# Kernel optimization log

Measured on AMD Instinct MI355X. Metric: run time of the kernel, lower is better.

The kernel has to match this reference:

```python
import jax, jax.numpy as jnp
import numpy as np

D = 128      # feature_dim
EMO = 25     # emotion_dim
DMM = 58     # _3dmm_dim
T = 512      # sequence length
BS = 16      # speaker batch
REP = 4      # repeat_interleave
NL = 3       # lstm layers
P_WEIGHT = 1e-5


def _lin(key, out_d, in_d):
    k1, k2 = jax.random.split(key)
    s = 1.0 / np.sqrt(in_d)
    W = jax.random.uniform(k1, (out_d, in_d), minval=-s, maxval=s, dtype=jnp.float32)
    b = jax.random.uniform(k2, (out_d,), minval=-s, maxval=s, dtype=jnp.float32)
    return W, b


def setup_inputs() -> dict:
    key = jax.random.key(0)
    ks = jax.random.split(key, 24)
    B = BS * REP
    inp = {
        'speaker_emotion': jax.random.normal(ks[0], (BS, T, EMO), jnp.float32),
        'listener_emotion': jax.random.normal(ks[1], (B, T, EMO), jnp.float32),
        'speaker_3dmm': jax.random.normal(ks[2], (BS, T, DMM), jnp.float32),
        'listener_3dmm': jax.random.normal(ks[3], (B, T, DMM), jnp.float32),
        'person_specific_factor': jax.random.normal(ks[4], (BS, D), jnp.float32),
        'repeat_interleave': REP,
    }
    specs = [('W_em', 'b_em', D, EMO), ('W_3d', 'b_3d', D, DMM),
             ('Wq_e', 'bq_e', D, D), ('Wk_e', 'bk_e', D, D), ('Wv_e', 'bv_e', D, D),
             ('Wq_d', 'bq_d', D, D), ('Wk_d', 'bk_d', D, D), ('Wv_d', 'bv_d', D, D),
             ('W_fus', 'b_fus', D, 2 * D), ('W_fc1', 'b_fc1', D, D), ('W_fc2', 'b_fc2', 1, D)]
    for i, (wn, bn, o, ii) in enumerate(specs):
        W, b = _lin(ks[5 + i], o, ii)
        inp[wn] = W
        inp[bn] = b
    # stacked 3-layer LSTM params, torch gate order (i, f, g, o)
    kL = jax.random.split(ks[5 + len(specs)], 4)
    s = 1.0 / np.sqrt(D)
    inp['W_ih'] = jax.random.uniform(kL[0], (NL, 4 * D, D), minval=-s, maxval=s, dtype=jnp.float32)
    inp['W_hh'] = jax.random.uniform(kL[1], (NL, 4 * D, D), minval=-s, maxval=s, dtype=jnp.float32)
    inp['b_ih'] = jax.random.uniform(kL[2], (NL, 4 * D), minval=-s, maxval=s, dtype=jnp.float32)
    inp['b_hh'] = jax.random.uniform(kL[3], (NL, 4 * D), minval=-s, maxval=s, dtype=jnp.float32)
    return inp


def _cross_attn(y, x, Wq, bq, Wk, bk, Wv, bv):
    # queries from listener features y [b,q,d]; keys/values from speaker x [b,k,d]
    q = y @ Wq.T + bq
    k = x @ Wk.T + bk
    v = x @ Wv.T + bv
    attn = jax.nn.softmax(jnp.einsum('bqd,bkd->bqk', q, k) / np.sqrt(D), axis=-1)
    return jnp.einsum('bqk,bkd->bqd', attn, v)


def _lstm_flat(flat, W_ih, W_hh, b_ih, b_hh):
    # faithful replication of the per-timestep torch loop: one 3-layer LSTM
    # over the flattened (t-major, b-minor) sequence, batch size 1.
    def step(carry, x):
        h, c = carry  # each [NL, D]
        new_h, new_c, inp = [], [], x
        for l in range(NL):
            g = inp @ W_ih[l].T + b_ih[l] + h[l] @ W_hh[l].T + b_hh[l]
            i, f, gg, o = jnp.split(g, 4)
            cc = jax.nn.sigmoid(f) * c[l] + jax.nn.sigmoid(i) * jnp.tanh(gg)
            hh = jax.nn.sigmoid(o) * jnp.tanh(cc)
            new_h.append(hh)
            new_c.append(cc)
            inp = hh
        return (jnp.stack(new_h), jnp.stack(new_c)), inp
    init = (jnp.zeros((NL, flat.shape[-1]), flat.dtype), jnp.zeros((NL, flat.shape[-1]), flat.dtype))
    _, outs = jax.lax.scan(step, init, flat)
    return outs  # [T*B, D]


def reference(speaker_emotion, listener_emotion, speaker_3dmm, listener_3dmm,
              person_specific_factor, W_em, b_em, W_3d, b_3d,
              Wq_e, bq_e, Wk_e, bk_e, Wv_e, bv_e,
              Wq_d, bq_d, Wk_d, bk_d, Wv_d, bv_d,
              W_fus, b_fus, W_fc1, b_fc1, W_fc2, b_fc2,
              W_ih, W_hh, b_ih, b_hh, repeat_interleave):
    r = repeat_interleave
    se = jnp.repeat(speaker_emotion, r, axis=0)
    sd = jnp.repeat(speaker_3dmm, r, axis=0)
    pf = jnp.repeat(person_specific_factor, r, axis=0)[:, None, :]  # [B,1,D]

    le = listener_emotion @ W_em.T + b_em
    se_enc = se @ W_em.T + b_em
    se_enc = jnp.concatenate([P_WEIGHT * pf, se_enc], axis=1)  # [B,T+1,D]
    emo_feat = _cross_attn(le, se_enc, Wq_e, bq_e, Wk_e, bk_e, Wv_e, bv_e)

    ld = listener_3dmm @ W_3d.T + b_3d
    sd_enc = sd @ W_3d.T + b_3d
    sd_enc = jnp.concatenate([P_WEIGHT * pf, sd_enc], axis=1)
    dmm_feat = _cross_attn(ld, sd_enc, Wq_d, bq_d, Wk_d, bk_d, Wv_d, bv_d)

    enc = jnp.concatenate([emo_feat, dmm_feat], axis=-1) @ W_fus.T + b_fus  # [B,T,D]
    B = enc.shape[0]
    flat = jnp.swapaxes(enc, 0, 1).reshape(-1, D)  # [T*B, D], t-major
    outs = _lstm_flat(flat, W_ih, W_hh, b_ih, b_hh)
    last = outs[-B:]  # outputs of the final torch lstm call, out[-1,:,:] -> [B,D]
    h = jax.nn.relu(last @ W_fc1.T + b_fc1)  # dropout is identity in eval
    return jax.nn.sigmoid(h @ W_fc2.T + b_fc2)  # [B,1]
```

## Files before the change

### kernel.cpp

```cpp
#include <hip/hip_runtime.h>

typedef unsigned int uint32;
typedef unsigned short uint16;

#define NSTEP 32768

__device__ __forceinline__ float rcp_(float x) {
#if __has_builtin(__builtin_amdgcn_rcpf)
  return __builtin_amdgcn_rcpf(x);
#else
  return 1.0f / x;
#endif
}
__device__ __forceinline__ float sigm_(float x) { return rcp_(1.0f + __expf(-x)); }
__device__ __forceinline__ float tanh_(float x) { return 1.0f - 2.0f * rcp_(1.0f + __expf(2.0f * x)); }

__device__ __forceinline__ float fdot2_(uint32 a, uint32 b, float c) {
#if __has_builtin(__builtin_amdgcn_fdot2)
  typedef _Float16 h2_t __attribute__((ext_vector_type(2)));
  return __builtin_amdgcn_fdot2(__builtin_bit_cast(h2_t, a), __builtin_bit_cast(h2_t, b), c, false);
#else
  float r;
  asm("v_dot2_f32_f16 %0, %1, %2, %3" : "=v"(r) : "v"(a), "v"(b), "v"(c));
  return r;
#endif
}
__device__ __forceinline__ uint16 f2h_(float x) { return __builtin_bit_cast(uint16, (_Float16)x); }

__device__ __forceinline__ uint32 aload_(uint32* p) {
  return __hip_atomic_load(p, __ATOMIC_RELAXED, __HIP_MEMORY_SCOPE_AGENT);
}
__device__ __forceinline__ uint32 aloadacq_(uint32* p) {
  return __hip_atomic_load(p, __ATOMIC_ACQUIRE, __HIP_MEMORY_SCOPE_AGENT);
}
__device__ __forceinline__ void astore_(uint32* p, uint32 v) {
  __hip_atomic_store(p, v, __ATOMIC_RELAXED, __HIP_MEMORY_SCOPE_AGENT);
}
__device__ __forceinline__ void astorerel_(uint32* p, uint32 v) {
  __hip_atomic_store(p, v, __ATOMIC_RELEASE, __HIP_MEMORY_SCOPE_AGENT);
}

__device__ __forceinline__ float addx1_(float x) {
  int y = __builtin_amdgcn_update_dpp(0, __builtin_bit_cast(int, x), 0xB1, 0xF, 0xF, true);
  return x + __builtin_bit_cast(float, y);
}
__device__ __forceinline__ float addx2_(float x) {
  int y = __builtin_amdgcn_update_dpp(0, __builtin_bit_cast(int, x), 0x4E, 0xF, 0xF, true);
  return x + __builtin_bit_cast(float, y);
}
__device__ __forceinline__ float addx16_(float x) {
  int y = __builtin_amdgcn_ds_swizzle(__builtin_bit_cast(int, x), 0x401F);
  return x + __builtin_bit_cast(float, y);
}

__global__ __launch_bounds__(64) void prep_kernel(const float* __restrict__ Wih,
                                                  const float* __restrict__ Whh,
                                                  uint32* __restrict__ wih16,
                                                  uint32* __restrict__ whh16,
                                                  uint32* __restrict__ flags) {
  int rg = blockIdx.x;
  int d = threadIdx.x;
  const float* src = (rg < 1536) ? Wih : Whh;
  uint32* dst = (rg < 1536) ? wih16 : whh16;
  int row = (rg < 1536) ? rg : rg - 1536;
  float a = src[row * 128 + 2 * d];
  float b = src[row * 128 + 2 * d + 1];
  dst[row * 64 + d] = (uint32)f2h_(a) | ((uint32)f2h_(b) << 16);
  if (rg == 0 && d < 4) flags[d] = 0;
}

__global__ __launch_bounds__(256) void kv_proj_kernel(
    const float* __restrict__ src, const float* __restrict__ pf,
    const float* __restrict__ Wemb, const float* __restrict__ bemb,
    const float* __restrict__ Wk, const float* __restrict__ bk,
    const float* __restrict__ Wv, const float* __restrict__ bv,
    float* __restrict__ K, float* __restrict__ V, int in_d) {
  int b = blockIdx.y;
  int s0 = blockIdx.x * 57;
  int tid = threadIdx.x;
  int bsrc = b >> 2;
  __shared__ __align__(16) float e_tile[57][128];
  __shared__ __align__(16) float s_tile[57][60];
  int nsrc = 57 * in_d;
  for (int idx = tid; idx < nsrc; idx += 256) {
    int r = idx / in_d, i = idx - r * in_d;
    int s = s0 + r;
    s_tile[r][i] = (s >= 1) ? src[((size_t)bsrc * 512 + (s - 1)) * in_d + i] : 0.0f;
  }
  __syncthreads();
  int j = tid & 127, half = tid >> 7;
  int r0 = half ? 28 : 0;
  {
    float acc[29];
    float bb = bemb[j];
#pragma unroll
    for (int r = 0; r < 29; ++r) acc[r] = bb;
    for (int i = 0; i < in_d; ++i) {
      float w = Wemb[j * in_d + i];
#pragma unroll
      for (int r = 0; r < 29; ++r) acc[r] += w * s_tile[r0 + r][i];
    }
#pragma unroll
    for (int r = 0; r < 29; ++r) {
      int s = s0 + r0 + r;
      e_tile[r0 + r][j] = (s == 0) ? (1e-5f * pf[(size_t)bsrc * 128 + j]) : acc[r];
    }
  }
  __syncthreads();
  {
    float acck[29], accv[29];
    float bkj = bk[j], bvj = bv[j];
#pragma unroll
    for (int r = 0; r < 29; ++r) { acck[r] = bkj; accv[r] = bvj; }
    for (int i = 0; i < 128; i += 4) {
      float4 wk = *(const float4*)&Wk[j * 128 + i];
      float4 wv = *(const float4*)&Wv[j * 128 + i];
#pragma unroll
      for (int r = 0; r < 29; ++r) {
        float4 e4 = *(const float4*)&e_tile[r0 + r][i];
        acck[r] += wk.x * e4.x + wk.y * e4.y + wk.z * e4.z + wk.w * e4.w;
        accv[r] += wv.x * e4.x + wv.y * e4.y + wv.z * e4.z + wv.w * e4.w;
      }
    }
#pragma unroll
    for (int r = 0; r < 29; ++r) {
      int s = s0 + r0 + r;
      K[((size_t)b * 513 + s) * 128 + j] = acck[r];
      V[((size_t)b * 513 + s) * 128 + j] = accv[r];
    }
  }
}

__global__ __launch_bounds__(256) void attn_kernel(
    const float* __restrict__ lst,
    const float* __restrict__ Wemb, const float* __restrict__ bemb,
    const float* __restrict__ Wq, const float* __restrict__ bq,
    const float* __restrict__ Kg, const float* __restrict__ Vg,
    float* __restrict__ feat, int in_d) {
  int b = blockIdx.y, qt = blockIdx.x;
  int tid = threadIdx.x;
  __shared__ __align__(16) float q_tile[64][132];
  __shared__ __align__(16) float k_tile[60][132];
  __shared__ __align__(16) float v_tile[60][132];
  __shared__ __align__(16) float p_tile[64][60];
  int nsrc = 64 * in_d;
  for (int idx = tid; idx < nsrc; idx += 256) {
    int r = idx / in_d, i = idx - r * in_d;
    p_tile[r][i] = lst[((size_t)b * 512 + qt * 64 + r) * in_d + i];
  }
  __syncthreads();
  int j = tid & 127, half = tid >> 7;
  int r0 = half * 32;
  {
    float acc[32];
    float bb = bemb[j];
#pragma unroll
    for (int r = 0; r < 32; ++r) acc[r] = bb;
    for (int i = 0; i < in_d; ++i) {
      float w = Wemb[j * in_d + i];
#pragma unroll
      for (int r = 0; r < 32; ++r) acc[r] += w * p_tile[r0 + r][i];
    }
#pragma unroll
    for (int r = 0; r < 32; ++r) k_tile[r0 + r][j] = acc[r];
  }
  __syncthreads();
  {
    float acc[32];
    float bb = bq[j];
#pragma unroll
    for (int r = 0; r < 32; ++r) acc[r] = bb;
    for (int i = 0; i < 128; i += 4) {
      float4 w4 = *(const float4*)&Wq[j * 128 + i];
#pragma unroll
      for (int r = 0; r < 32; ++r) {
        float4 e4 = *(const float4*)&k_tile[r0 + r][i];
        acc[r] += w4.x * e4.x + w4.y * e4.y + w4.z * e4.z + w4.w * e4.w;
      }
    }
#pragma unroll
    for (int r = 0; r < 32; ++r) q_tile[r0 + r][j] = acc[r];
  }
  int r = tid >> 2, c4 = tid & 3;
  float m = -1e30f, l = 0.0f;
  float o[8][4];
#pragma unroll
  for (int kk = 0; kk < 8; ++kk)
#pragma unroll
    for (int x = 0; x < 4; ++x) o[kk][x] = 0.0f;
  const float SCALE = 0.08838834764831845f;
  for (int kt = 0; kt < 9; ++kt) {
    __syncthreads();
    for (int idx = tid; idx < 57 * 32; idx += 256) {
      int rr = idx >> 5, cc = idx & 31;
      *(float4*)&k_tile[rr][cc * 4] = *(const float4*)&Kg[((size_t)b * 513 + kt * 57 + rr) * 128 + cc * 4];
      *(float4*)&v_tile[rr][cc * 4] = *(const float4*)&Vg[((size_t)b * 513 + kt * 57 + rr) * 128 + cc * 4];
    }
    __syncthreads();
    float s[15];
#pragma unroll
    for (int jj = 0; jj < 15; ++jj) s[jj] = 0.0f;
    for (int i = 0; i < 128; i += 4) {
      float4 q4 = *(const float4*)&q_tile[r][i];
#pragma unroll
      for (int jj = 0; jj < 15; ++jj) {
        float4 k4 = *(const float4*)&k_tile[c4 + jj * 4][i];
        s[jj] += q4.x * k4.x + q4.y * k4.y + q4.z * k4.z + q4.w * k4.w;
      }
    }
    float tmax = -1e30f;
#pragma unroll
    for (int jj = 0; jj < 15; ++jj) {
      int jcol = c4 + jj * 4;
      s[jj] = (jcol < 57) ? s[jj] * SCALE : -1e30f;
      tmax = fmaxf(tmax, s[jj]);
    }
    tmax = fmaxf(tmax, __shfl_xor(tmax, 1));
    tmax = fmaxf(tmax, __shfl_xor(tmax, 2));
    float mnew = fmaxf(m, tmax);
    float corr = __expf(m - mnew);
    float psum = 0.0f;
#pragma unroll
    for (int jj = 0; jj < 15; ++jj) {
      float p = __expf(s[jj] - mnew);
      psum += p;
      p_tile[r][c4 + jj * 4] = p;
    }
    psum += __shfl_xor(psum, 1);
    psum += __shfl_xor(psum, 2);
    l = l * corr + psum;
    m = mnew;
#pragma unroll
    for (int kk = 0; kk < 8; ++kk)
#pragma unroll
      for (int x = 0; x < 4; ++x) o[kk][x] *= corr;
    __syncthreads();
    for (int jcol = 0; jcol < 57; ++jcol) {
      float p = p_tile[r][jcol];
#pragma unroll
      for (int kk = 0; kk < 8; ++kk) {
        float4 v4 = *(const float4*)&v_tile[jcol][c4 * 4 + kk * 16];
        o[kk][0] += p * v4.x; o[kk][1] += p * v4.y; o[kk][2] += p * v4.z; o[kk][3] += p * v4.w;
      }
    }
  }
  float rl = 1.0f / l;
#pragma unroll
  for (int kk = 0; kk < 8; ++kk) {
    float4 st;
    st.x = o[kk][0] * rl; st.y = o[kk][1] * rl; st.z = o[kk][2] * rl; st.w = o[kk][3] * rl;
    *(float4*)&feat[((size_t)b * 512 + qt * 64 + r) * 128 + c4 * 4 + kk * 16] = st;
  }
}

__global__ __launch_bounds__(256) void fuse_kernel(
    const float* __restrict__ fe, const float* __restrict__ fd,
    const float* __restrict__ Wfus, const float* __restrict__ bfus,
    uint16* __restrict__ flat16) {
  int b = blockIdx.y, tt = blockIdx.x;
  int tid = threadIdx.x;
  __shared__ __align__(16) float f_tile[64][260];
  for (int idx = tid; idx < 64 * 32; idx += 256) {
    int r = idx >> 5, c = idx & 31;
    *(float4*)&f_tile[r][c * 4] = *(const float4*)&fe[((size_t)b * 512 + tt * 64 + r) * 128 + c * 4];
    *(float4*)&f_tile[r][128 + c * 4] = *(const float4*)&fd[((size_t)b * 512 + tt * 64 + r) * 128 + c * 4];
  }
  __syncthreads();
  int j = tid & 127, half = tid >> 7;
  int r0 = half * 32;
  float acc[32];
  float bb = bfus[j];
#pragma unroll
  for (int r = 0; r < 32; ++r) acc[r] = bb;
  for (int i = 0; i < 256; i += 4) {
    float4 w4 = *(const float4*)&Wfus[j * 256 + i];
#pragma unroll
    for (int r = 0; r < 32; ++r) {
      float4 e4 = *(const float4*)&f_tile[r0 + r][i];
      acc[r] += w4.x * e4.x + w4.y * e4.y + w4.z * e4.z + w4.w * e4.w;
    }
  }
#pragma unroll
  for (int r = 0; r < 32; ++r) {
    int t = tt * 64 + r0 + r;
    flat16[((size_t)t * 64 + b) * 128 + j] = f2h_(acc[r]);
  }
}

__global__ __launch_bounds__(512, 2) void lstm_kernel(
    const uint32* __restrict__ wih16, const uint32* __restrict__ whh16,
    const float* __restrict__ bih, const float* __restrict__ bhh,
    const uint32* __restrict__ flat16,
    uint32* hand32, uint32* flags,
    float* __restrict__ outs64) {
  const int z = blockIdx.x;
  const int j = threadIdx.x;
  const int L = j & 63, w = j >> 6;
  const int kk = (L & 3) | ((L >> 2) & 4);
  const int rr = ((L >> 2) & 3) | (((L >> 5) & 1) << 2);
  const bool kb0 = (L & 1) != 0, kb1 = (L & 2) != 0, kb2 = (L & 16) != 0;
  __shared__ __align__(16) uint32 h16[64];
  __shared__ __align__(16) float act[512];
  uint4 wih[16], whh[16];
#pragma unroll
  for (int a = 0; a < 8; ++a) {
    int R = (w << 6) + (rr << 3) + a;
    const uint32* p = &wih16[((size_t)z * 512 + R) * 64 + (kk << 3)];
    wih[2 * a] = *(const uint4*)p;
    wih[2 * a + 1] = *(const uint4*)(p + 4);
    const uint32* q = &whh16[((size_t)z * 512 + R) * 64 + (kk << 3)];
    whh[2 * a] = *(const uint4*)q;
    whh[2 * a + 1] = *(const uint4*)(q + 4);
  }
  const int myrow = (w << 6) + (rr << 3) + kk;
  const float bcv = bih[(size_t)z * 512 + myrow] + bhh[(size_t)z * 512 + myrow];
  float c0 = 0.0f, c1 = 0.0f;
  if (j < 64) h16[j] = 0;
  __syncthreads();
  const size_t HSTR = (size_t)(NSTEP + 8) * 64;
  const uint32* xsrc = (z == 0) ? flat16 : hand32 + (size_t)(z - 1) * HSTR;
  uint32* hdst = hand32 + (size_t)z * HSTR;
  uint32* flagA = (z > 0) ? &flags[z - 1] : (uint32*)0;
  uint32 Fc = 0;
  if (z > 0) { while (Fc < 1u) Fc = aloadacq_(flagA); }
  uint4 xa = *(const uint4*)(xsrc + (kk << 3));
  uint4 xb = *(const uint4*)(xsrc + (kk << 3) + 4);
  float acc[8];
#pragma unroll
  for (int a = 0; a < 8; ++a) {
    float v = 0.0f;
    v = fdot2_(wih[2 * a].x, xa.x, v); v = fdot2_(wih[2 * a].y, xa.y, v);
    v = fdot2_(wih[2 * a].z, xa.z, v); v = fdot2_(wih[2 * a].w, xa.w, v);
    v = fdot2_(wih[2 * a + 1].x, xb.x, v); v = fdot2_(wih[2 * a + 1].y, xb.y, v);
    v = fdot2_(wih[2 * a + 1].z, xb.z, v); v = fdot2_(wih[2 * a + 1].w, xb.w, v);
    acc[a] = v;
  }
  for (int t = 0; t < NSTEP; ++t) {
    if (z > 0 && t + 2 <= NSTEP) {
      while (Fc < (uint32)(t + 2)) Fc = aloadacq_(flagA);
    }
    const uint32* xp = xsrc + (size_t)(t + 1) * 64 + (kk << 3);
    xa = *(const uint4*)xp;
    xb = *(const uint4*)(xp + 4);
    {
      uint4 ha = *(const uint4*)&h16[kk << 3];
      uint4 hb = *(const uint4*)&h16[(kk << 3) + 4];
#pragma unroll
      for (int a = 0; a < 8; ++a) {
        float v = acc[a];
        v = fdot2_(whh[2 * a].x, ha.x, v); v = fdot2_(whh[2 * a].y, ha.y, v);
        v = fdot2_(whh[2 * a].z, ha.z, v); v = fdot2_(whh[2 * a].w, ha.w, v);
        v = fdot2_(whh[2 * a + 1].x, hb.x, v); v = fdot2_(whh[2 * a + 1].y, hb.y, v);
        v = fdot2_(whh[2 * a + 1].z, hb.z, v); v = fdot2_(whh[2 * a + 1].w, hb.w, v);
        acc[a] = v;
      }
    }
#pragma unroll
    for (int a = 0; a < 8; ++a) acc[a] = addx1_(acc[a]);
#pragma unroll
    for (int a = 0; a < 8; ++a) acc[a] = addx2_(acc[a]);
#pragma unroll
    for (int a = 0; a < 8; ++a) acc[a] = addx16_(acc[a]);
    float s01 = kb0 ? acc[1] : acc[0];
    float s23 = kb0 ? acc[3] : acc[2];
    float s45 = kb0 ? acc[5] : acc[4];
    float s67 = kb0 ? acc[7] : acc[6];
    float s0123 = kb1 ? s23 : s01;
    float s4567 = kb1 ? s67 : s45;
    float g = (kb2 ? s4567 : s0123) + bcv;
    float av = (w == 4 || w == 5) ? tanh_(g) : sigm_(g);
    act[(w << 6) + (rr << 3) + kk] = av;
    __syncthreads();
    if (j < 64) {
      float2 ia = *(const float2*)&act[2 * j];
      float2 fa = *(const float2*)&act[2 * j + 128];
      float2 ga = *(const float2*)&act[2 * j + 256];
      float2 oa = *(const float2*)&act[2 * j + 384];
      c0 = fa.x * c0 + ia.x * ga.x;
      c1 = fa.y * c1 + ia.y * ga.y;
      float h0 = oa.x * tanh_(c0);
      float h1 = oa.y * tanh_(c1);
      uint32 u = (uint32)f2h_(h0) | ((uint32)f2h_(h1) << 16);
      h16[j] = u;
      if (z < 2) {
        astore_(&hdst[(size_t)t * 64 + j], u);
        if ((t & 7) == 7) {
          asm volatile("s_waitcnt vmcnt(0)" ::: "memory");
          if (j == 0) astorerel_(&flags[z], (uint32)(t + 1));
        }
      } else if (t >= NSTEP - 64) {
        float2 st; st.x = h0; st.y = h1;
        *(float2*)&outs64[(size_t)(t - (NSTEP - 64)) * 128 + 2 * j] = st;
      }
    }
#pragma unroll
    for (int a = 0; a < 8; ++a) {
      float v = 0.0f;
      v = fdot2_(wih[2 * a].x, xa.x, v); v = fdot2_(wih[2 * a].y, xa.y, v);
      v = fdot2_(wih[2 * a].z, xa.z, v); v = fdot2_(wih[2 * a].w, xa.w, v);
      v = fdot2_(wih[2 * a + 1].x, xb.x, v); v = fdot2_(wih[2 * a + 1].y, xb.y, v);
      v = fdot2_(wih[2 * a + 1].z, xb.z, v); v = fdot2_(wih[2 * a + 1].w, xb.w, v);
      acc[a] = v;
    }
    __syncthreads();
  }
}

__global__ __launch_bounds__(128) void head_kernel(
    const float* __restrict__ outs64,
    const float* __restrict__ Wfc1, const float* __restrict__ bfc1,
    const float* __restrict__ Wfc2, const float* __restrict__ bfc2,
    float* __restrict__ out) {
  int j = threadIdx.x;
  __shared__ __align__(16) float hbuf[128];
  __shared__ float red[2];
  for (int b = 0; b < 64; ++b) {
    hbuf[j] = outs64[(size_t)b * 128 + j];
    __syncthreads();
    float acc = bfc1[j];
    for (int i = 0; i < 128; i += 4) {
      float4 w4 = *(const float4*)&Wfc1[j * 128 + i];
      float4 h4 = *(const float4*)&hbuf[i];
      acc += w4.x * h4.x + w4.y * h4.y + w4.z * h4.z + w4.w * h4.w;
    }
    float zz = fmaxf(acc, 0.0f) * Wfc2[j];
#pragma unroll
    for (int off = 32; off >= 1; off >>= 1) zz += __shfl_down(zz, off);
    if ((j & 63) == 0) red[j >> 6] = zz;
    __syncthreads();
    if (j == 0) out[b] = rcp_(1.0f + __expf(-(red[0] + red[1] + bfc2[0])));
    __syncthreads();
  }
}

extern "C" void kernel_launch(void* const* d_in, const int* in_sizes, int n_in,
                              void* d_out, int out_size, void* d_ws, size_t ws_size,
                              hipStream_t stream) {
  const float* sp_emo = (const float*)d_in[0];
  const float* ls_emo = (const float*)d_in[1];
  const float* sp_dmm = (const float*)d_in[2];
  const float* ls_dmm = (const float*)d_in[3];
  const float* pf = (const float*)d_in[4];
  const float* W_em = (const float*)d_in[6];  const float* b_em = (const float*)d_in[7];
  const float* W_3d = (const float*)d_in[8];  const float* b_3d = (const float*)d_in[9];
  const float* Wq_e = (const float*)d_in[10]; const float* bq_e = (const float*)d_in[11];
  const float* Wk_e = (const float*)d_in[12]; const float* bk_e = (const float*)d_in[13];
  const float* Wv_e = (const float*)d_in[14]; const float* bv_e = (const float*)d_in[15];
  const float* Wq_d = (const float*)d_in[16]; const float* bq_d = (const float*)d_in[17];
  const float* Wk_d = (const float*)d_in[18]; const float* bk_d = (const float*)d_in[19];
  const float* Wv_d = (const float*)d_in[20]; const float* bv_d = (const float*)d_in[21];
  const float* W_fus = (const float*)d_in[22]; const float* b_fus = (const float*)d_in[23];
  const float* W_fc1 = (const float*)d_in[24]; const float* b_fc1 = (const float*)d_in[25];
  const float* W_fc2 = (const float*)d_in[26]; const float* b_fc2 = (const float*)d_in[27];
  const float* W_ih = (const float*)d_in[28]; const float* W_hh = (const float*)d_in[29];
  const float* b_ih = (const float*)d_in[30]; const float* b_hh = (const float*)d_in[31];

  char* ws = (char*)d_ws;
  const size_t o_kvK = 0;
  const size_t o_kvV = 16809984;
  const size_t o_fe = 33619968;
  const size_t o_fd = 50397184;
  const size_t o_wih = 67174400;
  const size_t o_whh = 67567616;
  const size_t o_flag = 67960832;
  const size_t o_outs = 67961088;

  float* Kbuf = (float*)(ws + o_kvK);
  float* Vbuf = (float*)(ws + o_kvV);
  float* febuf = (float*)(ws + o_fe);
  float* fdbuf = (float*)(ws + o_fd);
  uint16* flatbuf = (uint16*)(ws + o_kvV);
  uint32* wih16 = (uint32*)(ws + o_wih);
  uint32* whh16 = (uint32*)(ws + o_whh);
  uint32* flags = (uint32*)(ws + o_flag);
  float* outs64 = (float*)(ws + o_outs);
  uint32* hand32 = (uint32*)(ws + o_kvK);

  prep_kernel<<<3072, 64, 0, stream>>>(W_ih, W_hh, wih16, whh16, flags);
  kv_proj_kernel<<<dim3(9, 64), 256, 0, stream>>>(sp_emo, pf, W_em, b_em, Wk_e, bk_e, Wv_e, bv_e, Kbuf, Vbuf, 25);
  attn_kernel<<<dim3(8, 64), 256, 0, stream>>>(ls_emo, W_em, b_em, Wq_e, bq_e, Kbuf, Vbuf, febuf, 25);
  kv_proj_kernel<<<dim3(9, 64), 256, 0, stream>>>(sp_dmm, pf, W_3d, b_3d, Wk_d, bk_d, Wv_d, bv_d, Kbuf, Vbuf, 58);
  attn_kernel<<<dim3(8, 64), 256, 0, stream>>>(ls_dmm, W_3d, b_3d, Wq_d, bq_d, Kbuf, Vbuf, fdbuf, 58);
  fuse_kernel<<<dim3(8, 64), 256, 0, stream>>>(febuf, fdbuf, W_fus, b_fus, flatbuf);
  lstm_kernel<<<3, 512, 0, stream>>>(wih16, whh16, b_ih, b_hh, (const uint32*)flatbuf, hand32, flags, outs64);
  head_kernel<<<1, 128, 0, stream>>>(outs64, W_fc1, b_fc1, W_fc2, b_fc2, (float*)d_out);
}
```

Before: 41.18 ms.

## Stage LSTM inputs through LDS double buffer with wavefront-0 flag polling

Each LSTM layer block now has only the first 64 threads load the next input vector, two steps ahead, into a shared double buffer. Previously all 512 threads issued per-step global uint4 loads. The spin-wait on the upstream layer's flag moves to a single thread, sits after the cell update and runs further ahead (t+4). Weight registers become named scalars instead of arrays, and launch bounds drop to one block per SM to relax register pressure. The intent is to cut redundant global traffic and flag polling from the serial recurrence, at the cost of extra LDS reads and subtler synchronisation ordering.

```diff
diff --git a/kernel.cpp b/kernel.cpp
--- a/kernel.cpp
+++ b/kernel.cpp
@@ -287,7 +287,7 @@
   }
 }
 
-__global__ __launch_bounds__(512, 2) void lstm_kernel(
+__global__ __launch_bounds__(512, 1) void lstm_kernel(
     const uint32* __restrict__ wih16, const uint32* __restrict__ whh16,
     const float* __restrict__ bih, const float* __restrict__ bhh,
     const uint32* __restrict__ flat16,
@@ -300,76 +300,84 @@
   const int rr = ((L >> 2) & 3) | (((L >> 5) & 1) << 2);
   const bool kb0 = (L & 1) != 0, kb1 = (L & 2) != 0, kb2 = (L & 16) != 0;
   __shared__ __align__(16) uint32 h16[64];
+  __shared__ __align__(16) uint32 xbuf[2][64];
   __shared__ __align__(16) float act[512];
-  uint4 wih[16], whh[16];
-#pragma unroll
-  for (int a = 0; a < 8; ++a) {
-    int R = (w << 6) + (rr << 3) + a;
-    const uint32* p = &wih16[((size_t)z * 512 + R) * 64 + (kk << 3)];
-    wih[2 * a] = *(const uint4*)p;
-    wih[2 * a + 1] = *(const uint4*)(p + 4);
-    const uint32* q = &whh16[((size_t)z * 512 + R) * 64 + (kk << 3)];
-    whh[2 * a] = *(const uint4*)q;
-    whh[2 * a + 1] = *(const uint4*)(q + 4);
-  }
+
+#define DECLW(a) uint4 wiA##a, wiB##a, whA##a, whB##a;
+  DECLW(0) DECLW(1) DECLW(2) DECLW(3) DECLW(4) DECLW(5) DECLW(6) DECLW(7)
+#undef DECLW
+#define LOADW(a) { const int R = (w << 6) + (rr << 3) + a; \
+    const uint32* p = &wih16[((size_t)z * 512 + R) * 64 + (kk << 3)]; \
+    wiA##a = *(const uint4*)p; wiB##a = *(const uint4*)(p + 4); \
+    const uint32* q = &whh16[((size_t)z * 512 + R) * 64 + (kk << 3)]; \
+    whA##a = *(const uint4*)q; whB##a = *(const uint4*)(q + 4); }
+  LOADW(0) LOADW(1) LOADW(2) LOADW(3) LOADW(4) LOADW(5) LOADW(6) LOADW(7)
+#undef LOADW
   const int myrow = (w << 6) + (rr << 3) + kk;
   const float bcv = bih[(size_t)z * 512 + myrow] + bhh[(size_t)z * 512 + myrow];
   float c0 = 0.0f, c1 = 0.0f;
-  if (j < 64) h16[j] = 0;
-  __syncthreads();
+
   const size_t HSTR = (size_t)(NSTEP + 8) * 64;
   const uint32* xsrc = (z == 0) ? flat16 : hand32 + (size_t)(z - 1) * HSTR;
   uint32* hdst = hand32 + (size_t)z * HSTR;
   uint32* flagA = (z > 0) ? &flags[z - 1] : (uint32*)0;
   uint32 Fc = 0;
-  if (z > 0) { while (Fc < 1u) Fc = aloadacq_(flagA); }
-  uint4 xa = *(const uint4*)(xsrc + (kk << 3));
-  uint4 xb = *(const uint4*)(xsrc + (kk << 3) + 4);
-  float acc[8];
-#pragma unroll
-  for (int a = 0; a < 8; ++a) {
-    float v = 0.0f;
-    v = fdot2_(wih[2 * a].x, xa.x, v); v = fdot2_(wih[2 * a].y, xa.y, v);
-    v = fdot2_(wih[2 * a].z, xa.z, v); v = fdot2_(wih[2 * a].w, xa.w, v);
-    v = fdot2_(wih[2 * a + 1].x, xb.x, v); v = fdot2_(wih[2 * a + 1].y, xb.y, v);
-    v = fdot2_(wih[2 * a + 1].z, xb.z, v); v = fdot2_(wih[2 * a + 1].w, xb.w, v);
-    acc[a] = v;
-  }
+
+  if (j < 64) {
+    if (z > 0 && j == 0) { while (Fc < 3u) Fc = aloadacq_(flagA); }
+    uint32 x0, x1;
+    if (z == 0) { x0 = xsrc[j]; x1 = xsrc[64 + j]; }
+    else { x0 = aload_((uint32*)&xsrc[j]); x1 = aload_((uint32*)&xsrc[64 + j]); }
+    xbuf[0][j] = x0; xbuf[1][j] = x1;
+    h16[j] = 0;
+  }
+  __syncthreads();
+
+  float acc0, acc1, acc2, acc3, acc4, acc5, acc6, acc7;
+#define IHDOT(a) { float v = 0.0f; \
+    v = fdot2_(wiA##a.x, xa.x, v); v = fdot2_(wiA##a.y, xa.y, v); \
+    v = fdot2_(wiA##a.z, xa.z, v); v = fdot2_(wiA##a.w, xa.w, v); \
+    v = fdot2_(wiB##a.x, xb.x, v); v = fdot2_(wiB##a.y, xb.y, v); \
+    v = fdot2_(wiB##a.z, xb.z, v); v = fdot2_(wiB##a.w, xb.w, v); \
+    acc##a = v; }
+#define HHDOT(a) { float v = acc##a; \
+    v = fdot2_(whA##a.x, ha.x, v); v = fdot2_(whA##a.y, ha.y, v); \
+    v = fdot2_(whA##a.z, ha.z, v); v = fdot2_(whA##a.w, ha.w, v); \
+    v = fdot2_(whB##a.x, hb.x, v); v = fdot2_(whB##a.y, hb.y, v); \
+    v = fdot2_(whB##a.z, hb.z, v); v = fdot2_(whB##a.w, hb.w, v); \
+    acc##a = v; }
+  {
+    uint4 xa = *(const uint4*)&xbuf[0][kk << 3];
+    uint4 xb = *(const uint4*)&xbuf[0][(kk << 3) + 4];
+    IHDOT(0) IHDOT(1) IHDOT(2) IHDOT(3) IHDOT(4) IHDOT(5) IHDOT(6) IHDOT(7)
+  }
+
   for (int t = 0; t < NSTEP; ++t) {
-    if (z > 0 && t + 2 <= NSTEP) {
-      while (Fc < (uint32)(t + 2)) Fc = aloadacq_(flagA);
-    }
-    const uint32* xp = xsrc + (size_t)(t + 1) * 64 + (kk << 3);
-    xa = *(const uint4*)xp;
-    xb = *(const uint4*)(xp + 4);
+    uint32 xv = 0;
+    if (j < 64) {
+      const size_t xi = (size_t)(t + 2) * 64 + j;
+      xv = (z == 0) ? xsrc[xi] : aload_((uint32*)&xsrc[xi]);
+    }
     {
       uint4 ha = *(const uint4*)&h16[kk << 3];
       uint4 hb = *(const uint4*)&h16[(kk << 3) + 4];
-#pragma unroll
-      for (int a = 0; a < 8; ++a) {
-        float v = acc[a];
-        v = fdot2_(whh[2 * a].x, ha.x, v); v = fdot2_(whh[2 * a].y, ha.y, v);
-        v = fdot2_(whh[2 * a].z, ha.z, v); v = fdot2_(whh[2 * a].w, ha.w, v);
-        v = fdot2_(whh[2 * a + 1].x, hb.x, v); v = fdot2_(whh[2 * a + 1].y, hb.y, v);
-        v = fdot2_(whh[2 * a + 1].z, hb.z, v); v = fdot2_(whh[2 * a + 1].w, hb.w, v);
-        acc[a] = v;
-      }
-    }
-#pragma unroll
-    for (int a = 0; a < 8; ++a) acc[a] = addx1_(acc[a]);
-#pragma unroll
-    for (int a = 0; a < 8; ++a) acc[a] = addx2_(acc[a]);
-#pragma unroll
-    for (int a = 0; a < 8; ++a) acc[a] = addx16_(acc[a]);
-    float s01 = kb0 ? acc[1] : acc[0];
-    float s23 = kb0 ? acc[3] : acc[2];
-    float s45 = kb0 ? acc[5] : acc[4];
-    float s67 = kb0 ? acc[7] : acc[6];
+      HHDOT(0) HHDOT(1) HHDOT(2) HHDOT(3) HHDOT(4) HHDOT(5) HHDOT(6) HHDOT(7)
+    }
+    acc0 = addx1_(acc0); acc1 = addx1_(acc1); acc2 = addx1_(acc2); acc3 = addx1_(acc3);
+    acc4 = addx1_(acc4); acc5 = addx1_(acc5); acc6 = addx1_(acc6); acc7 = addx1_(acc7);
+    acc0 = addx2_(acc0); acc1 = addx2_(acc1); acc2 = addx2_(acc2); acc3 = addx2_(acc3);
+    acc4 = addx2_(acc4); acc5 = addx2_(acc5); acc6 = addx2_(acc6); acc7 = addx2_(acc7);
+    acc0 = addx16_(acc0); acc1 = addx16_(acc1); acc2 = addx16_(acc2); acc3 = addx16_(acc3);
+    acc4 = addx16_(acc4); acc5 = addx16_(acc5); acc6 = addx16_(acc6); acc7 = addx16_(acc7);
+    float s01 = kb0 ? acc1 : acc0;
+    float s23 = kb0 ? acc3 : acc2;
+    float s45 = kb0 ? acc5 : acc4;
+    float s67 = kb0 ? acc7 : acc6;
     float s0123 = kb1 ? s23 : s01;
     float s4567 = kb1 ? s67 : s45;
     float g = (kb2 ? s4567 : s0123) + bcv;
     float av = (w == 4 || w == 5) ? tanh_(g) : sigm_(g);
-    act[(w << 6) + (rr << 3) + kk] = av;
+    act[myrow] = av;
     __syncthreads();
     if (j < 64) {
       float2 ia = *(const float2*)&act[2 * j];
@@ -392,18 +400,22 @@
         float2 st; st.x = h0; st.y = h1;
         *(float2*)&outs64[(size_t)(t - (NSTEP - 64)) * 128 + 2 * j] = st;
       }
-    }
-#pragma unroll
-    for (int a = 0; a < 8; ++a) {
-      float v = 0.0f;
-      v = fdot2_(wih[2 * a].x, xa.x, v); v = fdot2_(wih[2 * a].y, xa.y, v);
-      v = fdot2_(wih[2 * a].z, xa.z, v); v = fdot2_(wih[2 * a].w, xa.w, v);
-      v = fdot2_(wih[2 * a + 1].x, xb.x, v); v = fdot2_(wih[2 * a + 1].y, xb.y, v);
-      v = fdot2_(wih[2 * a + 1].z, xb.z, v); v = fdot2_(wih[2 * a + 1].w, xb.w, v);
-      acc[a] = v;
-    }
-    __syncthreads();
-  }
+      xbuf[t & 1][j] = xv;
+      if (z > 0 && j == 0) {
+        const uint32 tgt = (t + 4 <= NSTEP) ? (uint32)(t + 4) : (uint32)NSTEP;
+        while (Fc < tgt) Fc = aloadacq_(flagA);
+      }
+    }
+    {
+      const uint32* xp = &xbuf[(t + 1) & 1][0];
+      uint4 xa = *(const uint4*)&xp[kk << 3];
+      uint4 xb = *(const uint4*)&xp[(kk << 3) + 4];
+      IHDOT(0) IHDOT(1) IHDOT(2) IHDOT(3) IHDOT(4) IHDOT(5) IHDOT(6) IHDOT(7)
+    }
+    __syncthreads();
+  }
+#undef IHDOT
+#undef HHDOT
 }
 
 __global__ __launch_bounds__(128) void head_kernel(
```

After: 36.27 ms. -11.9%, faster.
